# Performance work log

Hardware: AMD Instinct MI355X
Metric: run time of the kernel (lower is better)

Reference implementation:

```python
import jax, jax.numpy as jnp
import numpy as np

BLOCK_H = 32  # block_h from init
BLOCK_W = 32  # block_w from init


def _block_pool(mask, bh, bw):
    # mask: [H, S, S] int -> block mask [H, S//bh, S//bw] bool
    # Equivalent to the grouped Conv2d with all-ones kernel, stride=(bh,bw), then >0.
    H, S1, S2 = mask.shape
    m = mask.reshape(H, S1 // bh, bh, S2 // bw, bw).astype(jnp.float32)
    return m.sum(axis=(2, 4)) > 0


def _expand_block_mask(bm, bh, bw):
    # bm: [H, Nb_r, Nb_c] bool -> element mask [H, S, S] bool
    H, nr, nc = bm.shape
    e = jnp.broadcast_to(bm[:, :, None, :, None], (H, nr, bh, nc, bw))
    return e.reshape(H, nr * bh, nc * bw)


def setup_inputs() -> dict:
    key = jax.random.key(0)
    kq, kk, kv, km = jax.random.split(key, 4)
    Z, H, S, D = 1, 16, 2048, 64
    query = jax.random.normal(kq, (Z, H, S, D), dtype=jnp.float32)
    key_t = jax.random.normal(kk, (Z, H, S, D), dtype=jnp.float32)
    value = jax.random.normal(kv, (Z, H, S, D), dtype=jnp.float32)
    mask = jax.random.randint(km, (H, S, S), 0, 2, dtype=jnp.int32)
    return {"query": query, "key": key_t, "value": value, "mask": mask}


def reference(query, key, value, mask):
    # Dense equivalent of: sdd QK^T on layout blocks -> blocksparse causal
    # softmax (scale=1.0) -> dsd AV. Rows with no active blocks yield zeros,
    # matching the blocksparse representation (absent blocks contribute 0).
    H, S, _ = mask.shape
    bm = _block_pool(mask, BLOCK_H, BLOCK_W)              # [H, Nb, Nb]
    elem = _expand_block_mask(bm, BLOCK_H, BLOCK_W)       # [H, S, S]
    causal = jnp.tril(jnp.ones((S, S), dtype=bool))       # is_causal=True
    full = elem & causal                                  # [H, S, S]
    scale = 1.0                                           # scale=1.0 in forward

    scores = jnp.einsum('zhqd,zhkd->zhqk', query, key) * scale
    neg = jnp.asarray(-1e30, dtype=scores.dtype)
    scores = jnp.where(full[None], scores, neg)
    probs = jax.nn.softmax(scores, axis=-1)
    row_valid = jnp.any(full, axis=-1)                    # [H, S]
    probs = jnp.where(row_valid[None, :, :, None], probs, 0.0)
    out = jnp.einsum('zhqk,zhkd->zhqd', probs, value)
    return out
```

## Files before the change

kernel.cpp:

```cpp
#include <hip/hip_runtime.h>
#include <stdint.h>


#define HH 16
#define SS 2048
#define DD 64

using f32x4  = __attribute__((ext_vector_type(4))) float;
using s16x8  = __attribute__((ext_vector_type(8))) short;
using s16x4  = __attribute__((ext_vector_type(4))) short;
using bf16x8 = __attribute__((ext_vector_type(8))) __bf16;

#define AS1 __attribute__((address_space(1)))
#define AS3 __attribute__((address_space(3)))

__device__ __forceinline__ unsigned short f2bf(float f) {
  unsigned u = __builtin_bit_cast(unsigned, f);
  u += 0x7fffu + ((u >> 16) & 1u);
  return (unsigned short)(u >> 16);
}
__device__ __forceinline__ float bf2f(unsigned short u) {
  return __builtin_bit_cast(float, ((unsigned)u) << 16);
}

template <int CTRL>
__device__ __forceinline__ float dpp_step(float x) {
  int y = __builtin_amdgcn_update_dpp(__builtin_bit_cast(int, x),
                                      __builtin_bit_cast(int, x),
                                      CTRL, 0xF, 0xF, false);
  return __builtin_bit_cast(float, y);
}
__device__ __forceinline__ float row16_sum(float x) {
  x += dpp_step<0xB1>(x);
  x += dpp_step<0x4E>(x);
  x += dpp_step<0x141>(x);
  x += dpp_step<0x140>(x);
  return x;
}

__global__ __launch_bounds__(256) void prep_kernel(
    const int* __restrict__ mask, const float* __restrict__ K,
    const float* __restrict__ V, unsigned char* __restrict__ bmask,
    unsigned short* __restrict__ Khi, unsigned short* __restrict__ Klo,
    unsigned short* __restrict__ Vtb) {
  __shared__ float tile[64][65];
  const int wg = blockIdx.x;
  const int t  = threadIdx.x;
  if (wg < 256) {
    const int tid = wg * 256 + t;
    {
      const int h = tid >> 12, br = (tid >> 6) & 63, bc = tid & 63;
      const int4* p = (const int4*)(mask + ((size_t)(h * SS + br * 32) * SS + bc * 32));
      int acc = 0;
#pragma unroll
      for (int i = 0; i < 8; ++i) { int4 v = p[i]; acc |= v.x | v.y | v.z | v.w; }
      if (acc == 0) {
        for (int r = 1; r < 32; ++r) {
          const int4* q2 = (const int4*)(mask + ((size_t)(h * SS + br * 32 + r) * SS + bc * 32));
          int a2 = 0;
#pragma unroll
          for (int i = 0; i < 8; ++i) { int4 v = q2[i]; a2 |= v.x | v.y | v.z | v.w; }
          acc |= a2;
          if (acc) break;
        }
      }
      bmask[tid] = acc != 0 ? 1 : 0;
    }
    {
      const float4* K4 = (const float4*)K;
      ushort4* Kh4 = (ushort4*)Khi;
      ushort4* Kl4 = (ushort4*)Klo;
#pragma unroll
      for (int i = 0; i < 8; ++i) {
        float4 v = K4[(size_t)i * 65536 + tid];
        ushort4 hi, lo;
        hi.x = f2bf(v.x); lo.x = f2bf(v.x - bf2f(hi.x));
        hi.y = f2bf(v.y); lo.y = f2bf(v.y - bf2f(hi.y));
        hi.z = f2bf(v.z); lo.z = f2bf(v.z - bf2f(hi.z));
        hi.w = f2bf(v.w); lo.w = f2bf(v.w - bf2f(hi.w));
        Kh4[(size_t)i * 65536 + tid] = hi;
        Kl4[(size_t)i * 65536 + tid] = lo;
      }
    }
  } else {
    const int w2 = wg - 256;
    const int h = w2 >> 5, kt = w2 & 31;
    const float4* V4 = (const float4*)V;
#pragma unroll
    for (int j2 = 0; j2 < 4; ++j2) {
      int fi = t + j2 * 256;
      int row = fi >> 4, c4 = (fi & 15) * 4;
      float4 v = V4[(size_t)(h * SS + kt * 64 + row) * 16 + (fi & 15)];
      tile[row][c4] = v.x; tile[row][c4+1] = v.y; tile[row][c4+2] = v.z; tile[row][c4+3] = v.w;
    }
    __syncthreads();
    const int d = t >> 2, ks = (t & 3) * 16;
#pragma unroll
    for (int c = 0; c < 4; ++c) {
      ushort4 o;
      o.x = f2bf(tile[ks + c*4 + 0][d]);
      o.y = f2bf(tile[ks + c*4 + 1][d]);
      o.z = f2bf(tile[ks + c*4 + 2][d]);
      o.w = f2bf(tile[ks + c*4 + 3][d]);
      ((ushort4*)Vtb)[((size_t)(h * 64 + d) * SS + kt * 64 + ks + c*4) >> 2] = o;
    }
  }
}

__global__ __launch_bounds__(512, 1) void attn_kernel(
    const float* __restrict__ Q, const unsigned char* __restrict__ bmask,
    const unsigned short* __restrict__ Khi, const unsigned short* __restrict__ Klo,
    const unsigned short* __restrict__ Vtb, float* __restrict__ O) {
  const int id = blockIdx.x;
  const int h  = id & 15;
  const int p  = id >> 4;

  const int t    = threadIdx.x;
  const int wave = t >> 6, lane = t & 63;
  const int n16  = lane & 15, quad = lane >> 4;
  const int wsub = wave & 3;
  const int qb   = (wave < 4) ? p : (31 - p);
  const int lastkt = 31 - p;

  __shared__ __align__(16) short ldsKV[24576];
  __shared__ __align__(16) short ldsP[8][1088];

  const int srow = t >> 3;
  const int c8   = (t & 7) ^ (srow & 7);
  const unsigned short* gk = Khi + (size_t)h * SS * DD + srow * DD + c8 * 8;
  const unsigned short* gl = Klo + (size_t)h * SS * DD + srow * DD + c8 * 8;
  const unsigned short* gv = Vtb + ((size_t)(h * 64 + srow)) * SS + c8 * 8;
  const int lofs = t * 8;
  auto stage = [&](int kt, int buf) {
    short* kb = ldsKV + buf * 12288;
    __builtin_amdgcn_global_load_lds((const AS1 void*)(gk + kt * 4096),
                                     (AS3 void*)(kb + lofs), 16, 0, 0);
    __builtin_amdgcn_global_load_lds((const AS1 void*)(gl + kt * 4096),
                                     (AS3 void*)(kb + 4096 + lofs), 16, 0, 0);
    __builtin_amdgcn_global_load_lds((const AS1 void*)(gv + kt * 64),
                                     (AS3 void*)(kb + 8192 + lofs), 16, 0, 0);
  };

  const int qi0 = qb * 64 + wsub * 16;
  s16x8 qhi[2], qlo[2];
  {
    const float* qp = Q + ((size_t)(h * SS + qi0 + n16)) * DD + quad * 8;
#pragma unroll
    for (int kc = 0; kc < 2; ++kc) {
      float4 a = *(const float4*)(qp + kc * 32);
      float4 b = *(const float4*)(qp + kc * 32 + 4);
      float x[8] = {a.x, a.y, a.z, a.w, b.x, b.y, b.z, b.w};
      s16x8 fh, fl;
#pragma unroll
      for (int e = 0; e < 8; ++e) {
        unsigned short hi = f2bf(x[e]);
        fh[e] = (short)hi;
        fl[e] = (short)f2bf(x[e] - bf2f(hi));
      }
      qhi[kc] = fh; qlo[kc] = fl;
    }
  }

  const int qbr = qb * 2 + (wsub >> 1);
  const unsigned long long bmw = __ballot(bmask[(h << 12) + (qbr << 6) + lane] != 0);

  float l_i[4];
  f32x4 oa[4];
#pragma unroll
  for (int r = 0; r < 4; ++r) l_i[r] = 0.f;
#pragma unroll
  for (int db = 0; db < 4; ++db) oa[db] = f32x4{0.f, 0.f, 0.f, 0.f};

  stage(0, 0);
  for (int kt = 0; kt <= lastkt; ++kt) {
    __syncthreads();
    if (kt < lastkt) stage(kt + 1, (kt + 1) & 1);

    if (kt <= qb) {
      const short* khb = ldsKV + (kt & 1) * 12288;
      const short* klb = khb + 4096;
      const short* vbase = khb + 8192;

      f32x4 S[4];
#pragma unroll
      for (int nb = 0; nb < 4; ++nb) S[nb] = f32x4{0.f, 0.f, 0.f, 0.f};
#pragma unroll
      for (int kc = 0; kc < 2; ++kc) {
        bf16x8 ah = __builtin_bit_cast(bf16x8, qhi[kc]);
        bf16x8 al8 = __builtin_bit_cast(bf16x8, qlo[kc]);
#pragma unroll
        for (int nb = 0; nb < 4; ++nb) {
          int row = nb * 16 + n16;
          int pc  = (kc * 4 + quad) ^ (row & 7);
          bf16x8 kh = __builtin_bit_cast(bf16x8, *(const s16x8*)(khb + row * 64 + pc * 8));
          bf16x8 kl = __builtin_bit_cast(bf16x8, *(const s16x8*)(klb + row * 64 + pc * 8));
          S[nb] = __builtin_amdgcn_mfma_f32_16x16x32_bf16(ah, kh, S[nb], 0, 0, 0);
          S[nb] = __builtin_amdgcn_mfma_f32_16x16x32_bf16(al8, kh, S[nb], 0, 0, 0);
          S[nb] = __builtin_amdgcn_mfma_f32_16x16x32_bf16(ah, kl, S[nb], 0, 0, 0);
        }
      }

      const int b0 = (int)((bmw >> (kt * 2)) & 1ull);
      const int b1 = (int)((bmw >> (kt * 2 + 1)) & 1ull);
      if ((kt == qb) | !(b0 & b1)) {
#pragma unroll
        for (int nb = 0; nb < 4; ++nb) {
          int kj = kt * 64 + nb * 16 + n16;
          int bb = (nb < 2) ? b0 : b1;
#pragma unroll
          for (int r = 0; r < 4; ++r) {
            int qi = qi0 + quad * 4 + r;
            bool ok = (kj <= qi) && (bb != 0);
            S[nb][r] = ok ? S[nb][r] : -__builtin_inff();
          }
        }
      }

#pragma unroll
      for (int nb = 0; nb < 4; ++nb) {
#pragma unroll
        for (int r = 0; r < 4; ++r) {
          float pv = __expf(S[nb][r]);
          unsigned short pq = f2bf(pv);
          ldsP[wave][(quad * 4 + r) * 68 + nb * 16 + n16] = (short)pq;
          l_i[r] += bf2f(pq);
        }
      }

#pragma unroll
      for (int kc = 0; kc < 2; ++kc) {
        const short* pp = &ldsP[wave][n16 * 68 + kc * 32 + quad * 8];
        s16x4 x = *(const s16x4*)pp;
        s16x4 y = *(const s16x4*)(pp + 4);
        s16x8 pf8 = {x[0], x[1], x[2], x[3], y[0], y[1], y[2], y[3]};
        bf16x8 ap = __builtin_bit_cast(bf16x8, pf8);
#pragma unroll
        for (int db = 0; db < 4; ++db) {
          int row = db * 16 + n16;
          int pc  = (kc * 4 + quad) ^ (n16 & 7);
          s16x8 vv = *(const s16x8*)(vbase + row * 64 + pc * 8);
          oa[db] = __builtin_amdgcn_mfma_f32_16x16x32_bf16(
              ap, __builtin_bit_cast(bf16x8, vv), oa[db], 0, 0, 0);
        }
      }
    }
  }

  {
    float* op = O + ((size_t)(h * SS + qi0)) * DD;
#pragma unroll
    for (int r = 0; r < 4; ++r) {
      int qrow = quad * 4 + r;
      float lsum = row16_sum(l_i[r]);
      float inv = lsum > 0.f ? 1.f / lsum : 0.f;
#pragma unroll
      for (int db = 0; db < 4; ++db) {
        op[(size_t)qrow * DD + db * 16 + n16] = oa[db][r] * inv;
      }
    }
  }
}

extern "C" void kernel_launch(void* const* d_in, const int* in_sizes, int n_in,
                              void* d_out, int out_size, void* d_ws, size_t ws_size,
                              hipStream_t stream) {
  const float* Q   = (const float*)d_in[0];
  const float* K   = (const float*)d_in[1];
  const float* V   = (const float*)d_in[2];
  const int* mask  = (const int*)d_in[3];
  float* out       = (float*)d_out;

  unsigned char* bmask = (unsigned char*)d_ws;
  unsigned short* Khi  = (unsigned short*)((char*)d_ws + 65536);
  unsigned short* Klo  = (unsigned short*)((char*)d_ws + 65536 + 4194304);
  unsigned short* Vtb  = (unsigned short*)((char*)d_ws + 65536 + 2 * 4194304);

  prep_kernel<<<768, 256, 0, stream>>>(mask, K, V, bmask, Khi, Klo, Vtb);
  attn_kernel<<<256, 512, 0, stream>>>(Q, bmask, Khi, Klo, Vtb, out);
}
```

Measured before the change: 360.3 us.

## Compute transposed S so P stays in registers for the PV MFMA

Swaps the operands of the QK^T MFMA so each lane holds scores for consecutive key positions of a single query row. That output layout matches the B operand of the 16x16x16 bf16 MFMA, so P feeds the PV product straight from registers. This removes the per-wave LDS staging buffer for P and its write/read round trip. The cost is twice as many PV MFMAs at half K depth and narrower 8-byte V reads from LDS. The epilogue now reduces the row sum with two shuffles and stores float4 vectors.

```diff
diff --git a/kernel.cpp b/kernel.cpp
--- a/kernel.cpp
+++ b/kernel.cpp
@@ -23,19 +23,8 @@
   return __builtin_bit_cast(float, ((unsigned)u) << 16);
 }
 
-template <int CTRL>
-__device__ __forceinline__ float dpp_step(float x) {
-  int y = __builtin_amdgcn_update_dpp(__builtin_bit_cast(int, x),
-                                      __builtin_bit_cast(int, x),
-                                      CTRL, 0xF, 0xF, false);
-  return __builtin_bit_cast(float, y);
-}
-__device__ __forceinline__ float row16_sum(float x) {
-  x += dpp_step<0xB1>(x);
-  x += dpp_step<0x4E>(x);
-  x += dpp_step<0x141>(x);
-  x += dpp_step<0x140>(x);
-  return x;
+__device__ __forceinline__ f32x4 mfma16bf16(s16x4 a, s16x4 b, f32x4 c) {
+  return __builtin_amdgcn_mfma_f32_16x16x16bf16_1k(a, b, c, 0, 0, 0);
 }
 
 __global__ __launch_bounds__(256) void prep_kernel(
@@ -123,7 +112,6 @@
   const int lastkt = 31 - p;
 
   __shared__ __align__(16) short ldsKV[24576];
-  __shared__ __align__(16) short ldsP[8][1088];
 
   const int srow = t >> 3;
   const int c8   = (t & 7) ^ (srow & 7);
@@ -164,12 +152,12 @@
   const int qbr = qb * 2 + (wsub >> 1);
   const unsigned long long bmw = __ballot(bmask[(h << 12) + (qbr << 6) + lane] != 0);
 
-  float l_i[4];
+  float l_i = 0.f;
   f32x4 oa[4];
 #pragma unroll
-  for (int r = 0; r < 4; ++r) l_i[r] = 0.f;
-#pragma unroll
-  for (int db = 0; db < 4; ++db) oa[db] = f32x4{0.f, 0.f, 0.f, 0.f};
+  for (int dt = 0; dt < 4; ++dt) oa[dt] = f32x4{0.f, 0.f, 0.f, 0.f};
+
+  const int qi = qi0 + n16;
 
   stage(0, 0);
   for (int kt = 0; kt <= lastkt; ++kt) {
@@ -186,17 +174,17 @@
       for (int nb = 0; nb < 4; ++nb) S[nb] = f32x4{0.f, 0.f, 0.f, 0.f};
 #pragma unroll
       for (int kc = 0; kc < 2; ++kc) {
-        bf16x8 ah = __builtin_bit_cast(bf16x8, qhi[kc]);
-        bf16x8 al8 = __builtin_bit_cast(bf16x8, qlo[kc]);
+        bf16x8 qh8 = __builtin_bit_cast(bf16x8, qhi[kc]);
+        bf16x8 ql8 = __builtin_bit_cast(bf16x8, qlo[kc]);
 #pragma unroll
         for (int nb = 0; nb < 4; ++nb) {
           int row = nb * 16 + n16;
           int pc  = (kc * 4 + quad) ^ (row & 7);
           bf16x8 kh = __builtin_bit_cast(bf16x8, *(const s16x8*)(khb + row * 64 + pc * 8));
           bf16x8 kl = __builtin_bit_cast(bf16x8, *(const s16x8*)(klb + row * 64 + pc * 8));
-          S[nb] = __builtin_amdgcn_mfma_f32_16x16x32_bf16(ah, kh, S[nb], 0, 0, 0);
-          S[nb] = __builtin_amdgcn_mfma_f32_16x16x32_bf16(al8, kh, S[nb], 0, 0, 0);
-          S[nb] = __builtin_amdgcn_mfma_f32_16x16x32_bf16(ah, kl, S[nb], 0, 0, 0);
+          S[nb] = __builtin_amdgcn_mfma_f32_16x16x32_bf16(kh, qh8, S[nb], 0, 0, 0);
+          S[nb] = __builtin_amdgcn_mfma_f32_16x16x32_bf16(kh, ql8, S[nb], 0, 0, 0);
+          S[nb] = __builtin_amdgcn_mfma_f32_16x16x32_bf16(kl, qh8, S[nb], 0, 0, 0);
         }
       }
 
@@ -205,12 +193,11 @@
       if ((kt == qb) | !(b0 & b1)) {
 #pragma unroll
         for (int nb = 0; nb < 4; ++nb) {
-          int kj = kt * 64 + nb * 16 + n16;
           int bb = (nb < 2) ? b0 : b1;
+          int k0 = kt * 64 + nb * 16 + quad * 4;
 #pragma unroll
           for (int r = 0; r < 4; ++r) {
-            int qi = qi0 + quad * 4 + r;
-            bool ok = (kj <= qi) && (bb != 0);
+            bool ok = (k0 + r <= qi) && (bb != 0);
             S[nb][r] = ok ? S[nb][r] : -__builtin_inff();
           }
         }
@@ -218,45 +205,36 @@
 
 #pragma unroll
       for (int nb = 0; nb < 4; ++nb) {
+        s16x4 pb;
 #pragma unroll
         for (int r = 0; r < 4; ++r) {
           float pv = __expf(S[nb][r]);
           unsigned short pq = f2bf(pv);
-          ldsP[wave][(quad * 4 + r) * 68 + nb * 16 + n16] = (short)pq;
-          l_i[r] += bf2f(pq);
-        }
-      }
-
-#pragma unroll
-      for (int kc = 0; kc < 2; ++kc) {
-        const short* pp = &ldsP[wave][n16 * 68 + kc * 32 + quad * 8];
-        s16x4 x = *(const s16x4*)pp;
-        s16x4 y = *(const s16x4*)(pp + 4);
-        s16x8 pf8 = {x[0], x[1], x[2], x[3], y[0], y[1], y[2], y[3]};
-        bf16x8 ap = __builtin_bit_cast(bf16x8, pf8);
-#pragma unroll
-        for (int db = 0; db < 4; ++db) {
-          int row = db * 16 + n16;
-          int pc  = (kc * 4 + quad) ^ (n16 & 7);
-          s16x8 vv = *(const s16x8*)(vbase + row * 64 + pc * 8);
-          oa[db] = __builtin_amdgcn_mfma_f32_16x16x32_bf16(
-              ap, __builtin_bit_cast(bf16x8, vv), oa[db], 0, 0, 0);
+          pb[r] = (short)pq;
+          l_i += bf2f(pq);
+        }
+#pragma unroll
+        for (int dt = 0; dt < 4; ++dt) {
+          int row = dt * 16 + n16;
+          int cc  = ((nb * 2) + (quad >> 1)) ^ (row & 7);
+          s16x4 vv = *(const s16x4*)(vbase + row * 64 + cc * 8 + (quad & 1) * 4);
+          oa[dt] = mfma16bf16(vv, pb, oa[dt]);
         }
       }
     }
   }
 
   {
-    float* op = O + ((size_t)(h * SS + qi0)) * DD;
-#pragma unroll
-    for (int r = 0; r < 4; ++r) {
-      int qrow = quad * 4 + r;
-      float lsum = row16_sum(l_i[r]);
-      float inv = lsum > 0.f ? 1.f / lsum : 0.f;
-#pragma unroll
-      for (int db = 0; db < 4; ++db) {
-        op[(size_t)qrow * DD + db * 16 + n16] = oa[db][r] * inv;
-      }
+    float lsum = l_i;
+    lsum += __shfl_xor(lsum, 16);
+    lsum += __shfl_xor(lsum, 32);
+    float inv = lsum > 0.f ? 1.f / lsum : 0.f;
+    float* op = O + ((size_t)(h * SS + qi)) * DD + quad * 4;
+#pragma unroll
+    for (int dt = 0; dt < 4; ++dt) {
+      f32x4 o = oa[dt];
+      float4 st = {o[0] * inv, o[1] * inv, o[2] * inv, o[3] * inv};
+      *(float4*)(op + dt * 16) = st;
     }
   }
 }
```

After: 350.2 us. 1.03x faster.
